# Kernel optimization log

Measured on AMD Instinct MI355X. Metric: run time of the kernel, lower is better.

The kernel has to match this reference:

```python
import jax, jax.numpy as jnp
import numpy as np

N_DRUG = 572
D = 512
K = 64          # neighbor_sample_size
T = 30000       # tail entities
R = 200         # relations
MAX_DEG = 32    # padded invariant_adj neighbor count
EPS = 1e-5


def setup_inputs() -> dict:
    key = jax.random.key(0)
    ks = jax.random.split(key, 10)
    return {
        "drug_embed_W": jax.random.normal(ks[0], (N_DRUG, D), jnp.float32),
        "rela_embed_W": jax.random.normal(ks[1], (R, D), jnp.float32),
        "ent_embed_W": jax.random.normal(ks[2], (T, D), jnp.float32),
        "Wa": jax.random.normal(ks[3], (D, D), jnp.float32) / np.float32(np.sqrt(D)),
        "lin_W": jax.random.normal(ks[4], (2 * D, D), jnp.float32) / np.float32(np.sqrt(2 * D)),
        "lin_b": jnp.zeros((D,), jnp.float32),
        "gamma": jnp.ones((D,), jnp.float32),
        "beta": jnp.zeros((D,), jnp.float32),
        "drug_name": jnp.arange(N_DRUG, dtype=jnp.int64 if jax.config.jax_enable_x64 else jnp.int32),
        "adj_tail": jax.random.randint(ks[5], (N_DRUG, K), 0, T),
        "adj_relation": jax.random.randint(ks[6], (N_DRUG, K), 0, R),
        "nbr_idx": jax.random.randint(ks[7], (N_DRUG, MAX_DEG), 0, N_DRUG),
        "nbr_deg": jax.random.randint(ks[8], (N_DRUG,), 0, MAX_DEG),
        "epoch": 2,
    }


def _forward(drug_embed_W, rela_embed_W, ent_embed_W, Wa, lin_W, lin_b, gamma, beta,
             drug_name, adj_tail, adj_relation, nbr_idx, nbr_deg, epoch):
    drug_e = drug_embed_W[drug_name]          # [N, D]
    rela = rela_embed_W[adj_relation]         # [N, K, D]
    ent = ent_embed_W[adj_tail]               # [N, K, D]

    # relation-aware attention over sampled neighbors (AttentionLayer)
    q = drug_e @ Wa                           # [N, D]
    scores = jnp.einsum('nd,nkd->nk', q, rela) * (1.0 / np.float32(np.sqrt(D)))
    attn = jax.nn.softmax(scores, axis=1)     # [N, K]
    agg = jnp.einsum('nk,nkd->nd', attn, ent) # [N, D]

    # Linear1: Linear(2D->D) + ReLU + BatchNorm1d (training-mode batch stats)
    h = jnp.concatenate([agg, drug_e], axis=1) @ lin_W + lin_b
    h = jax.nn.relu(h)
    mean = jnp.mean(h, axis=0)
    var = jnp.var(h, axis=0)                  # biased, as torch BN normalization
    drug_f = (h - mean) * jax.lax.rsqrt(var + EPS) * gamma + beta

    if epoch > 1:
        # sequential per-node neighbor-mean smoothing (in-place semantics)
        mask = (jnp.arange(MAX_DEG)[None, :] < nbr_deg[:, None])  # [N, MAX_DEG]

        def step(f, i):
            pos = nbr_idx[i]
            m = mask[i][:, None].astype(f.dtype)
            s = jnp.sum(f[pos] * m, axis=0)
            deg = nbr_deg[i]
            avg = s / jnp.maximum(deg, 1).astype(f.dtype)
            new = jnp.where(deg > 0, (avg + f[i]) * 0.5, f[i])
            return f.at[i].set(new), None

        drug_f, _ = jax.lax.scan(step, drug_f, jnp.arange(N_DRUG))
    return drug_f


def reference(drug_embed_W, rela_embed_W, ent_embed_W, Wa, lin_W, lin_b, gamma, beta,
              drug_name, adj_tail, adj_relation, nbr_idx, nbr_deg, epoch):
    return _forward(drug_embed_W, rela_embed_W, ent_embed_W, Wa, lin_W, lin_b, gamma, beta,
                    drug_name, adj_tail, adj_relation, nbr_idx, nbr_deg, epoch)
```

## Files before the change

kernel.cpp:

```cpp
#include <hip/hip_runtime.h>

#define N_DRUG 572
#define DIM 512
#define KNBR 64
#define MAXDEG 32
#define FS 17
#define MN (N_DRUG * DIM)
#define LSTR 68

__global__ __launch_bounds__(256) void gemm_kernel(
    const float* __restrict__ drugW, const int* __restrict__ drug_name,
    const float* __restrict__ agg, const float* __restrict__ B,
    float* __restrict__ C, int M, int Kc, int mode)
{
    __shared__ float As[2][32 * LSTR];
    __shared__ float Bs[2][32 * LSTR];
    const int t   = threadIdx.x;
    const int tn  = t & 15, tm = t >> 4;
    const int arow = t & 63, akq = (t >> 6) * 8;
    const int brow = t >> 3, bcq = (t & 7) * 8;
    const int c0  = blockIdx.x * 64;
    const int r0  = blockIdx.y * 64;
    const int ks0 = blockIdx.z * Kc;
    const int nsteps = Kc >> 5;
    const int row = r0 + arow;
    const bool aval = row < M;
    const int dn = aval ? drug_name[row] : 0;
    const float* __restrict__ drow = drugW + (size_t)dn * 512;
    const float* __restrict__ grow = agg + (size_t)row * 512;

    float av[8], bv[8];
    float acc[4][4] = {{0.f}};

    {
        const int k = ks0 + akq;
        if (aval) {
            const float* src = (mode == 1) ? ((k < 512) ? (grow + k) : (drow + (k - 512)))
                                           : (drow + k);
            const float4 x = ((const float4*)src)[0];
            const float4 y = ((const float4*)src)[1];
            av[0]=x.x; av[1]=x.y; av[2]=x.z; av[3]=x.w;
            av[4]=y.x; av[5]=y.y; av[6]=y.z; av[7]=y.w;
        } else {
            #pragma unroll
            for (int j = 0; j < 8; ++j) av[j] = 0.f;
        }
        const float* bsrc = B + (size_t)(ks0 + brow) * 512 + c0 + bcq;
        const float4 x = ((const float4*)bsrc)[0];
        const float4 y = ((const float4*)bsrc)[1];
        bv[0]=x.x; bv[1]=x.y; bv[2]=x.z; bv[3]=x.w;
        bv[4]=y.x; bv[5]=y.y; bv[6]=y.z; bv[7]=y.w;
    }
    #pragma unroll
    for (int i = 0; i < 8; ++i) As[0][(akq + i) * LSTR + arow] = av[i];
    *(float4*)&Bs[0][brow * LSTR + bcq]     = make_float4(bv[0], bv[1], bv[2], bv[3]);
    *(float4*)&Bs[0][brow * LSTR + bcq + 4] = make_float4(bv[4], bv[5], bv[6], bv[7]);
    __syncthreads();

    int p = 0;
    for (int s = 0; s < nsteps; ++s) {
        const bool more = (s + 1) < nsteps;
        if (more) {
            const int k = ks0 + (s + 1) * 32 + akq;
            if (aval) {
                const float* src = (mode == 1) ? ((k < 512) ? (grow + k) : (drow + (k - 512)))
                                               : (drow + k);
                const float4 x = ((const float4*)src)[0];
                const float4 y = ((const float4*)src)[1];
                av[0]=x.x; av[1]=x.y; av[2]=x.z; av[3]=x.w;
                av[4]=y.x; av[5]=y.y; av[6]=y.z; av[7]=y.w;
            }
            const float* bsrc = B + (size_t)(ks0 + (s + 1) * 32 + brow) * 512 + c0 + bcq;
            const float4 x = ((const float4*)bsrc)[0];
            const float4 y = ((const float4*)bsrc)[1];
            bv[0]=x.x; bv[1]=x.y; bv[2]=x.z; bv[3]=x.w;
            bv[4]=y.x; bv[5]=y.y; bv[6]=y.z; bv[7]=y.w;
        }
        #pragma unroll
        for (int kk = 0; kk < 32; ++kk) {
            const float4 a = *(const float4*)&As[p][kk * LSTR + tm * 4];
            const float4 b = *(const float4*)&Bs[p][kk * LSTR + tn * 4];
            const float ar[4] = {a.x, a.y, a.z, a.w};
            const float br[4] = {b.x, b.y, b.z, b.w};
            #pragma unroll
            for (int i = 0; i < 4; ++i)
                #pragma unroll
                for (int j = 0; j < 4; ++j)
                    acc[i][j] = fmaf(ar[i], br[j], acc[i][j]);
        }
        __syncthreads();
        if (more) {
            const int q2 = p ^ 1;
            #pragma unroll
            for (int i = 0; i < 8; ++i) As[q2][(akq + i) * LSTR + arow] = av[i];
            *(float4*)&Bs[q2][brow * LSTR + bcq]     = make_float4(bv[0], bv[1], bv[2], bv[3]);
            *(float4*)&Bs[q2][brow * LSTR + bcq + 4] = make_float4(bv[4], bv[5], bv[6], bv[7]);
            __syncthreads();
            p = q2;
        }
    }

    float* __restrict__ Cp = C + (size_t)blockIdx.z * MN;
    #pragma unroll
    for (int i = 0; i < 4; ++i) {
        const int r = r0 + tm * 4 + i;
        if (r < M)
            *(float4*)&Cp[(size_t)r * 512 + c0 + tn * 4] =
                make_float4(acc[i][0], acc[i][1], acc[i][2], acc[i][3]);
    }
}

__global__ __launch_bounds__(256) void attn_kernel(
    const float* __restrict__ relaW, const float* __restrict__ entW,
    const int* __restrict__ adj_tail, const int* __restrict__ adj_rel,
    const float* __restrict__ q, int skq, float* __restrict__ agg)
{
    const int n = blockIdx.x;
    const int t = threadIdx.x;
    const int lane = t & 63;
    const int w = t >> 6;
    __shared__ float sc[64];
    __shared__ int tails[64];
    __shared__ int rels[64];
    if (t < 64) { tails[t] = adj_tail[n * 64 + t]; rels[t] = adj_rel[n * 64 + t]; }

    float qv[8];
    {
        const float* qp = q + (size_t)n * 512 + lane * 8;
        float4 x = ((const float4*)qp)[0], y = ((const float4*)qp)[1];
        qv[0]=x.x; qv[1]=x.y; qv[2]=x.z; qv[3]=x.w;
        qv[4]=y.x; qv[5]=y.y; qv[6]=y.z; qv[7]=y.w;
        if (skq == 2) {
            const float* qp2 = qp + MN;
            float4 x2 = ((const float4*)qp2)[0], y2 = ((const float4*)qp2)[1];
            qv[0]+=x2.x; qv[1]+=x2.y; qv[2]+=x2.z; qv[3]+=x2.w;
            qv[4]+=y2.x; qv[5]+=y2.y; qv[6]+=y2.z; qv[7]+=y2.w;
        }
    }
    __syncthreads();

    #pragma unroll 4
    for (int kk = 0; kk < 16; ++kk) {
        const int k = w * 16 + kk;
        const float4* p = (const float4*)(relaW + (size_t)rels[k] * 512 + lane * 8);
        float4 x = p[0], y = p[1];
        float s = 0.f;
        s = fmaf(qv[0], x.x, s); s = fmaf(qv[1], x.y, s);
        s = fmaf(qv[2], x.z, s); s = fmaf(qv[3], x.w, s);
        s = fmaf(qv[4], y.x, s); s = fmaf(qv[5], y.y, s);
        s = fmaf(qv[6], y.z, s); s = fmaf(qv[7], y.w, s);
        #pragma unroll
        for (int off = 32; off >= 1; off >>= 1) s += __shfl_xor(s, off, 64);
        if (lane == 0) sc[k] = s * 0.0441941738241592f;
    }
    __syncthreads();

    if (w == 0) {
        float s = sc[lane];
        float m = s;
        #pragma unroll
        for (int off = 32; off >= 1; off >>= 1) m = fmaxf(m, __shfl_xor(m, off, 64));
        const float e = __expf(s - m);
        float sum = e;
        #pragma unroll
        for (int off = 32; off >= 1; off >>= 1) sum += __shfl_xor(sum, off, 64);
        sc[lane] = e / sum;
    }
    __syncthreads();

    float a0 = 0.f, a1 = 0.f;
    const int d2 = t * 2;
    #pragma unroll 8
    for (int k = 0; k < 64; ++k) {
        const float ak = sc[k];
        const float2 u = *(const float2*)(entW + (size_t)tails[k] * 512 + d2);
        a0 = fmaf(ak, u.x, a0);
        a1 = fmaf(ak, u.y, a1);
    }
    ((float2*)(agg + (size_t)n * 512))[t] = make_float2(a0, a1);
}

__global__ __launch_bounds__(512) void scan_kernel(
    float* hout, const float* __restrict__ hsrc, int nh,
    const float* __restrict__ linb,
    const float* __restrict__ gamma, const float* __restrict__ beta,
    const int* __restrict__ nbr_idx, const int* __restrict__ nbr_deg,
    const int* __restrict__ epoch)
{
    __shared__ float fs[(N_DRUG + 1) * FS];
    __shared__ int   offs[N_DRUG * MAXDEG];
    __shared__ float2 ivw[N_DRUG];
    __shared__ int   mxs[N_DRUG];
    __shared__ float part[2][32][16];
    __shared__ float bnp[2][16];
    __shared__ int   genext[2];
    __shared__ int   ge0s;

    const int t  = threadIdx.x;
    const int c  = t & 15;
    const int h  = (t >> 4) & 1;
    const int j  = t >> 5;
    const int rr = t >> 4;
    const int c0 = blockIdx.x * 16;

    for (int i = t; i < N_DRUG; i += 512) {
        const int d = nbr_deg[i];
        ivw[i] = (d > 0) ? make_float2(0.5f / (float)d, 0.5f) : make_float2(0.f, 1.f);
        const int4* np = (const int4*)&nbr_idx[i * MAXDEG];
        int4* op = (int4*)&offs[i * MAXDEG];
        int mx = -1;
        #pragma unroll
        for (int u = 0; u < 8; ++u) {
            int4 qq = np[u];
            const int b = u * 4;
            qq.x = (b + 0 < d) ? qq.x : N_DRUG;
            qq.y = (b + 1 < d) ? qq.y : N_DRUG;
            qq.z = (b + 2 < d) ? qq.z : N_DRUG;
            qq.w = (b + 3 < d) ? qq.w : N_DRUG;
            mx = max(mx, (qq.x < i) ? qq.x : -1);
            mx = max(mx, (qq.y < i) ? qq.y : -1);
            mx = max(mx, (qq.z < i) ? qq.z : -1);
            mx = max(mx, (qq.w < i) ? qq.w : -1);
            op[u] = qq;
        }
        mxs[i] = mx;
    }

    {
        const float bb = linb[c0 + c];
        float sl = 0.f, ql = 0.f;
        for (int r = rr; r < N_DRUG; r += 32) {
            const float* hp = hsrc + (size_t)r * DIM + c0 + c;
            float v = hp[0];
            for (int pt = 1; pt < nh; ++pt) v += hp[(size_t)pt * MN];
            v = fmaxf(v + bb, 0.f);
            fs[r * FS + c] = v;
            sl += v;
            ql = fmaf(v, v, ql);
        }
        part[0][rr][c] = sl;
        part[1][rr][c] = ql;
    }
    if (t < FS) fs[N_DRUG * FS + t] = 0.f;
    __syncthreads();

    if (t < 16) {
        float s = 0.f, sq = 0.f;
        #pragma unroll
        for (int k = 0; k < 32; ++k) { s += part[0][k][t]; sq += part[1][k][t]; }
        const float mean = s * (1.f / N_DRUG);
        const float var = sq * (1.f / N_DRUG) - mean * mean;
        const float rstd = rsqrtf(var + 1e-5f);
        const float scl = gamma[c0 + t] * rstd;
        bnp[0][t] = scl;
        bnp[1][t] = beta[c0 + t] - mean * scl;
    }
    if ((t >> 6) == 7) {
        const int l = t & 63;
        const int jj = 1 + l;
        const bool flag = (l >= 15) || (jj >= N_DRUG) || (mxs[min(jj, N_DRUG - 1)] >= 0);
        const unsigned long long b = __ballot(flag) & 0xFFFFULL;
        if (l == 0) ge0s = 1 + (int)__builtin_ctzll(b);
    }
    __syncthreads();

    {
        const float scl = bnp[0][c];
        const float shf = bnp[1][c];
        for (int r = rr; r < N_DRUG; r += 32)
            fs[r * FS + c] = fmaf(fs[r * FS + c], scl, shf);
    }
    __syncthreads();

    if (epoch[0] > 1) {
        int gs = 0, ge = ge0s;
        int4 o0, o1, o2, o3;
        {
            const int4* p = (const int4*)&offs[min(j, N_DRUG - 1) * MAXDEG + h * 16];
            o0 = p[0]; o1 = p[1]; o2 = p[2]; o3 = p[3];
        }
        int par = 0;
        while (gs < N_DRUG) {
            const bool pred = (gs + j) < ge;
            float s0 = 0.f, s1 = 0.f, s2 = 0.f, s3 = 0.f;
#define GATH4(Q) { s0 += fs[Q.x * FS + c]; s1 += fs[Q.y * FS + c]; \
                   s2 += fs[Q.z * FS + c]; s3 += fs[Q.w * FS + c]; }
            if (pred) { GATH4(o0) GATH4(o1) GATH4(o2) GATH4(o3) }
#undef GATH4
            int4 n0, n1, n2, n3;
            {
                const int4* p = (const int4*)&offs[min(ge + j, N_DRUG - 1) * MAXDEG + h * 16];
                n0 = p[0]; n1 = p[1]; n2 = p[2]; n3 = p[3];
            }
            float nv = 0.f;
            if (pred) {
                const float cur = fs[(gs + j) * FS + c];
                const float2 iw = ivw[gs + j];
                float sh = (s0 + s1) + (s2 + s3);
                sh += __shfl_xor(sh, 16, 64);
                nv = fmaf(sh, iw.x, cur * iw.y);
            }
            if ((t >> 6) == 7) {
                const int l = t & 63;
                const int jj = ge + 1 + l;
                const bool flag = (l >= 15) || (jj >= N_DRUG) ||
                                  (mxs[min(jj, N_DRUG - 1)] >= ge);
                const unsigned long long b = __ballot(flag) & 0xFFFFULL;
                if (l == 0) genext[par] = ge + 1 + (int)__builtin_ctzll(b);
            }
            __syncthreads();
            if (pred && h == 0) fs[(gs + j) * FS + c] = nv;
            __syncthreads();
            gs = ge;
            ge = genext[par];
            par ^= 1;
            o0 = n0; o1 = n1; o2 = n2; o3 = n3;
        }
    }
    __syncthreads();

    for (int r = rr; r < N_DRUG; r += 32)
        hout[(size_t)r * DIM + c0 + c] = fs[r * FS + c];
}

extern "C" void kernel_launch(void* const* d_in, const int* in_sizes, int n_in,
                              void* d_out, int out_size, void* d_ws, size_t ws_size,
                              hipStream_t stream)
{
    const float* drugW = (const float*)d_in[0];
    const float* relaW = (const float*)d_in[1];
    const float* entW  = (const float*)d_in[2];
    const float* Wa    = (const float*)d_in[3];
    const float* linW  = (const float*)d_in[4];
    const float* linb  = (const float*)d_in[5];
    const float* gamma = (const float*)d_in[6];
    const float* beta  = (const float*)d_in[7];
    const int* drug_name = (const int*)d_in[8];
    const int* adj_tail  = (const int*)d_in[9];
    const int* adj_rel   = (const int*)d_in[10];
    const int* nbr_idx   = (const int*)d_in[11];
    const int* nbr_deg   = (const int*)d_in[12];
    const int* epoch     = (const int*)d_in[13];

    float* ws = (float*)d_ws;
    float* out = (float*)d_out;

    const bool big = ws_size >= (size_t)7 * MN * sizeof(float);
    const int skq = big ? 2 : 1;
    const int skh = big ? 4 : 1;
    float* q   = ws;
    float* agg = ws + (size_t)(big ? 2 : 1) * MN;
    float* hp  = big ? (ws + (size_t)3 * MN) : out;

    gemm_kernel<<<dim3(8, 9, skq), 256, 0, stream>>>(
        drugW, drug_name, nullptr, Wa, q, N_DRUG, 512 / skq, 0);
    attn_kernel<<<N_DRUG, 256, 0, stream>>>(
        relaW, entW, adj_tail, adj_rel, q, skq, agg);
    gemm_kernel<<<dim3(8, 9, skh), 256, 0, stream>>>(
        drugW, drug_name, agg, linW, hp, N_DRUG, 1024 / skh, 1);
    scan_kernel<<<32, 512, 0, stream>>>(
        out, hp, skh, linb, gamma, beta, nbr_idx, nbr_deg, epoch);
}
```

Measured before the change: 226.1 us.

## Fuse all stages into one persistent kernel with grid barriers

```diff
diff --git a/kernel.cpp b/kernel.cpp
--- a/kernel.cpp
+++ b/kernel.cpp
@@ -2,26 +2,50 @@
 
 #define N_DRUG 572
 #define DIM 512
-#define KNBR 64
 #define MAXDEG 32
-#define FS 17
 #define MN (N_DRUG * DIM)
 #define LSTR 68
-
-__global__ __launch_bounds__(256) void gemm_kernel(
+#define FSW 9
+#define NBLK 256
+
+struct GemmS { float As[2][32 * LSTR]; float Bs[2][32 * LSTR]; };
+struct AttnS { float sc[64]; int tails[64]; int rels[64]; };
+struct ScanS {
+    float fs[(N_DRUG + 1) * FSW];
+    float fspad[3];
+    alignas(16) unsigned short offs[N_DRUG * MAXDEG];
+    float inv[N_DRUG];
+    unsigned short mxs[N_DRUG];
+    float part[2][32][8];
+    float bnp[2][8];
+    int genext[2];
+    int ge0;
+};
+union SmemU { GemmS g; AttnS a; ScanS s; };
+
+__device__ __forceinline__ void gridbar(int* cnt, int id) {
+    __syncthreads();
+    if (threadIdx.x == 0) {
+        __hip_atomic_fetch_add(&cnt[id], 1, __ATOMIC_ACQ_REL, __HIP_MEMORY_SCOPE_AGENT);
+        while (__hip_atomic_load(&cnt[id], __ATOMIC_RELAXED, __HIP_MEMORY_SCOPE_AGENT) < NBLK)
+            __builtin_amdgcn_s_sleep(8);
+        __builtin_amdgcn_fence(__ATOMIC_ACQUIRE, "agent");
+    }
+    __syncthreads();
+}
+
+__device__ void gemm_tile(GemmS& g,
     const float* __restrict__ drugW, const int* __restrict__ drug_name,
     const float* __restrict__ agg, const float* __restrict__ B,
-    float* __restrict__ C, int M, int Kc, int mode)
+    float* __restrict__ C, int M, int Kc, int mode, int bx, int by, int bz)
 {
-    __shared__ float As[2][32 * LSTR];
-    __shared__ float Bs[2][32 * LSTR];
-    const int t   = threadIdx.x;
-    const int tn  = t & 15, tm = t >> 4;
+    __syncthreads();
+    const int t = threadIdx.x;
+    const int tn = t & 15, tm = t >> 4;
     const int arow = t & 63, akq = (t >> 6) * 8;
     const int brow = t >> 3, bcq = (t & 7) * 8;
-    const int c0  = blockIdx.x * 64;
-    const int r0  = blockIdx.y * 64;
-    const int ks0 = blockIdx.z * Kc;
+    const int c0 = bx * 64, r0 = by * 64;
+    const int ks0 = bz * Kc;
     const int nsteps = Kc >> 5;
     const int row = r0 + arow;
     const bool aval = row < M;
@@ -52,9 +76,9 @@
         bv[4]=y.x; bv[5]=y.y; bv[6]=y.z; bv[7]=y.w;
     }
     #pragma unroll
-    for (int i = 0; i < 8; ++i) As[0][(akq + i) * LSTR + arow] = av[i];
-    *(float4*)&Bs[0][brow * LSTR + bcq]     = make_float4(bv[0], bv[1], bv[2], bv[3]);
-    *(float4*)&Bs[0][brow * LSTR + bcq + 4] = make_float4(bv[4], bv[5], bv[6], bv[7]);
+    for (int i = 0; i < 8; ++i) g.As[0][(akq + i) * LSTR + arow] = av[i];
+    *(float4*)&g.Bs[0][brow * LSTR + bcq]     = make_float4(bv[0], bv[1], bv[2], bv[3]);
+    *(float4*)&g.Bs[0][brow * LSTR + bcq + 4] = make_float4(bv[4], bv[5], bv[6], bv[7]);
     __syncthreads();
 
     int p = 0;
@@ -78,8 +102,8 @@
         }
         #pragma unroll
         for (int kk = 0; kk < 32; ++kk) {
-            const float4 a = *(const float4*)&As[p][kk * LSTR + tm * 4];
-            const float4 b = *(const float4*)&Bs[p][kk * LSTR + tn * 4];
+            const float4 a = *(const float4*)&g.As[p][kk * LSTR + tm * 4];
+            const float4 b = *(const float4*)&g.Bs[p][kk * LSTR + tn * 4];
             const float ar[4] = {a.x, a.y, a.z, a.w};
             const float br[4] = {b.x, b.y, b.z, b.w};
             #pragma unroll
@@ -92,15 +116,15 @@
         if (more) {
             const int q2 = p ^ 1;
             #pragma unroll
-            for (int i = 0; i < 8; ++i) As[q2][(akq + i) * LSTR + arow] = av[i];
-            *(float4*)&Bs[q2][brow * LSTR + bcq]     = make_float4(bv[0], bv[1], bv[2], bv[3]);
-            *(float4*)&Bs[q2][brow * LSTR + bcq + 4] = make_float4(bv[4], bv[5], bv[6], bv[7]);
+            for (int i = 0; i < 8; ++i) g.As[q2][(akq + i) * LSTR + arow] = av[i];
+            *(float4*)&g.Bs[q2][brow * LSTR + bcq]     = make_float4(bv[0], bv[1], bv[2], bv[3]);
+            *(float4*)&g.Bs[q2][brow * LSTR + bcq + 4] = make_float4(bv[4], bv[5], bv[6], bv[7]);
             __syncthreads();
             p = q2;
         }
     }
 
-    float* __restrict__ Cp = C + (size_t)blockIdx.z * MN;
+    float* __restrict__ Cp = C + (size_t)bz * MN;
     #pragma unroll
     for (int i = 0; i < 4; ++i) {
         const int r = r0 + tm * 4 + i;
@@ -110,29 +134,26 @@
     }
 }
 
-__global__ __launch_bounds__(256) void attn_kernel(
+__device__ void attn_one(AttnS& a,
     const float* __restrict__ relaW, const float* __restrict__ entW,
     const int* __restrict__ adj_tail, const int* __restrict__ adj_rel,
-    const float* __restrict__ q, int skq, float* __restrict__ agg)
+    const float* __restrict__ qb, int skq, float* __restrict__ agg, int n)
 {
-    const int n = blockIdx.x;
     const int t = threadIdx.x;
     const int lane = t & 63;
     const int w = t >> 6;
-    __shared__ float sc[64];
-    __shared__ int tails[64];
-    __shared__ int rels[64];
-    if (t < 64) { tails[t] = adj_tail[n * 64 + t]; rels[t] = adj_rel[n * 64 + t]; }
+    __syncthreads();
+    if (t < 64) { a.tails[t] = adj_tail[n * 64 + t]; a.rels[t] = adj_rel[n * 64 + t]; }
 
     float qv[8];
     {
-        const float* qp = q + (size_t)n * 512 + lane * 8;
+        const float* qp = qb + (size_t)n * 512 + lane * 8;
         float4 x = ((const float4*)qp)[0], y = ((const float4*)qp)[1];
         qv[0]=x.x; qv[1]=x.y; qv[2]=x.z; qv[3]=x.w;
         qv[4]=y.x; qv[5]=y.y; qv[6]=y.z; qv[7]=y.w;
-        if (skq == 2) {
-            const float* qp2 = qp + MN;
-            float4 x2 = ((const float4*)qp2)[0], y2 = ((const float4*)qp2)[1];
+        for (int pt = 1; pt < skq; ++pt) {
+            const float* q2 = qp + (size_t)pt * MN;
+            float4 x2 = ((const float4*)q2)[0], y2 = ((const float4*)q2)[1];
             qv[0]+=x2.x; qv[1]+=x2.y; qv[2]+=x2.z; qv[3]+=x2.w;
             qv[4]+=y2.x; qv[5]+=y2.y; qv[6]+=y2.z; qv[7]+=y2.w;
         }
@@ -142,7 +163,7 @@
     #pragma unroll 4
     for (int kk = 0; kk < 16; ++kk) {
         const int k = w * 16 + kk;
-        const float4* p = (const float4*)(relaW + (size_t)rels[k] * 512 + lane * 8);
+        const float4* p = (const float4*)(relaW + (size_t)a.rels[k] * 512 + lane * 8);
         float4 x = p[0], y = p[1];
         float s = 0.f;
         s = fmaf(qv[0], x.x, s); s = fmaf(qv[1], x.y, s);
@@ -151,12 +172,12 @@
         s = fmaf(qv[6], y.z, s); s = fmaf(qv[7], y.w, s);
         #pragma unroll
         for (int off = 32; off >= 1; off >>= 1) s += __shfl_xor(s, off, 64);
-        if (lane == 0) sc[k] = s * 0.0441941738241592f;
+        if (lane == 0) a.sc[k] = s * 0.0441941738241592f;
     }
     __syncthreads();
 
     if (w == 0) {
-        float s = sc[lane];
+        float s = a.sc[lane];
         float m = s;
         #pragma unroll
         for (int off = 32; off >= 1; off >>= 1) m = fmaxf(m, __shfl_xor(m, off, 64));
@@ -164,7 +185,7 @@
         float sum = e;
         #pragma unroll
         for (int off = 32; off >= 1; off >>= 1) sum += __shfl_xor(sum, off, 64);
-        sc[lane] = e / sum;
+        a.sc[lane] = e / sum;
     }
     __syncthreads();
 
@@ -172,155 +193,184 @@
     const int d2 = t * 2;
     #pragma unroll 8
     for (int k = 0; k < 64; ++k) {
-        const float ak = sc[k];
-        const float2 u = *(const float2*)(entW + (size_t)tails[k] * 512 + d2);
+        const float ak = a.sc[k];
+        const float2 u = *(const float2*)(entW + (size_t)a.tails[k] * 512 + d2);
         a0 = fmaf(ak, u.x, a0);
         a1 = fmaf(ak, u.y, a1);
     }
     ((float2*)(agg + (size_t)n * 512))[t] = make_float2(a0, a1);
 }
 
-__global__ __launch_bounds__(512) void scan_kernel(
-    float* hout, const float* __restrict__ hsrc, int nh,
-    const float* __restrict__ linb,
+__global__ __launch_bounds__(256, 1) void mega_kernel(
+    const float* __restrict__ drugW, const float* __restrict__ relaW,
+    const float* __restrict__ entW, const float* __restrict__ Wa,
+    const float* __restrict__ linW, const float* __restrict__ linb,
     const float* __restrict__ gamma, const float* __restrict__ beta,
-    const int* __restrict__ nbr_idx, const int* __restrict__ nbr_deg,
-    const int* __restrict__ epoch)
+    const int* __restrict__ drug_name, const int* __restrict__ adj_tail,
+    const int* __restrict__ adj_rel, const int* __restrict__ nbr_idx,
+    const int* __restrict__ nbr_deg, const int* __restrict__ epoch,
+    int skq, int skh, int* cnt, float* q, float* agg, float* hbuf,
+    float* __restrict__ out)
 {
-    __shared__ float fs[(N_DRUG + 1) * FS];
-    __shared__ int   offs[N_DRUG * MAXDEG];
-    __shared__ float2 ivw[N_DRUG];
-    __shared__ int   mxs[N_DRUG];
-    __shared__ float part[2][32][16];
-    __shared__ float bnp[2][16];
-    __shared__ int   genext[2];
-    __shared__ int   ge0s;
-
-    const int t  = threadIdx.x;
-    const int c  = t & 15;
-    const int h  = (t >> 4) & 1;
-    const int j  = t >> 5;
-    const int rr = t >> 4;
-    const int c0 = blockIdx.x * 16;
-
-    for (int i = t; i < N_DRUG; i += 512) {
-        const int d = nbr_deg[i];
-        ivw[i] = (d > 0) ? make_float2(0.5f / (float)d, 0.5f) : make_float2(0.f, 1.f);
-        const int4* np = (const int4*)&nbr_idx[i * MAXDEG];
-        int4* op = (int4*)&offs[i * MAXDEG];
-        int mx = -1;
-        #pragma unroll
-        for (int u = 0; u < 8; ++u) {
-            int4 qq = np[u];
-            const int b = u * 4;
-            qq.x = (b + 0 < d) ? qq.x : N_DRUG;
-            qq.y = (b + 1 < d) ? qq.y : N_DRUG;
-            qq.z = (b + 2 < d) ? qq.z : N_DRUG;
-            qq.w = (b + 3 < d) ? qq.w : N_DRUG;
-            mx = max(mx, (qq.x < i) ? qq.x : -1);
-            mx = max(mx, (qq.y < i) ? qq.y : -1);
-            mx = max(mx, (qq.z < i) ? qq.z : -1);
-            mx = max(mx, (qq.w < i) ? qq.w : -1);
-            op[u] = qq;
-        }
-        mxs[i] = mx;
-    }
-
+    __shared__ SmemU sm;
+    const int blk = blockIdx.x;
+    const int t = threadIdx.x;
+
+    for (int job = blk; job < 72 * skq; job += NBLK) {
+        const int bz = job / 72, rem = job % 72;
+        gemm_tile(sm.g, drugW, drug_name, q , Wa, q,
+                  N_DRUG, 512 / skq, 0, rem % 8, rem / 8, bz);
+    }
+    gridbar(cnt, 0);
+
+    for (int n = blk; n < N_DRUG; n += NBLK)
+        attn_one(sm.a, relaW, entW, adj_tail, adj_rel, q, skq, agg, n);
+    gridbar(cnt, 1);
+
+    for (int job = blk; job < 72 * skh; job += NBLK) {
+        const int bz = job / 72, rem = job % 72;
+        gemm_tile(sm.g, drugW, drug_name, agg, linW, hbuf,
+                  N_DRUG, 1024 / skh, 1, rem % 8, rem / 8, bz);
+    }
+    gridbar(cnt, 2);
+
+    if (blk >= 64) return;
+    __syncthreads();
     {
-        const float bb = linb[c0 + c];
-        float sl = 0.f, ql = 0.f;
-        for (int r = rr; r < N_DRUG; r += 32) {
-            const float* hp = hsrc + (size_t)r * DIM + c0 + c;
-            float v = hp[0];
-            for (int pt = 1; pt < nh; ++pt) v += hp[(size_t)pt * MN];
-            v = fmaxf(v + bb, 0.f);
-            fs[r * FS + c] = v;
-            sl += v;
-            ql = fmaf(v, v, ql);
-        }
-        part[0][rr][c] = sl;
-        part[1][rr][c] = ql;
-    }
-    if (t < FS) fs[N_DRUG * FS + t] = 0.f;
-    __syncthreads();
-
-    if (t < 16) {
-        float s = 0.f, sq = 0.f;
-        #pragma unroll
-        for (int k = 0; k < 32; ++k) { s += part[0][k][t]; sq += part[1][k][t]; }
-        const float mean = s * (1.f / N_DRUG);
-        const float var = sq * (1.f / N_DRUG) - mean * mean;
-        const float rstd = rsqrtf(var + 1e-5f);
-        const float scl = gamma[c0 + t] * rstd;
-        bnp[0][t] = scl;
-        bnp[1][t] = beta[c0 + t] - mean * scl;
-    }
-    if ((t >> 6) == 7) {
-        const int l = t & 63;
-        const int jj = 1 + l;
-        const bool flag = (l >= 15) || (jj >= N_DRUG) || (mxs[min(jj, N_DRUG - 1)] >= 0);
-        const unsigned long long b = __ballot(flag) & 0xFFFFULL;
-        if (l == 0) ge0s = 1 + (int)__builtin_ctzll(b);
-    }
-    __syncthreads();
-
-    {
-        const float scl = bnp[0][c];
-        const float shf = bnp[1][c];
+        ScanS& S = sm.s;
+        const int c8 = t & 7;
+        const int rr = t >> 3;
+        const int h  = (t >> 3) & 1;
+        const int j  = t >> 4;
+        const int c0 = blk * 8;
+
+        for (int i = t; i < N_DRUG; i += 256) {
+            const int d = nbr_deg[i];
+            S.inv[i] = (d > 0) ? 0.5f / (float)d : 0.f;
+            const int4* np = (const int4*)&nbr_idx[i * MAXDEG];
+            unsigned* op = (unsigned*)&S.offs[i * MAXDEG];
+            int mx = -1;
+            #pragma unroll
+            for (int u = 0; u < 8; ++u) {
+                int4 qq = np[u];
+                const int b = u * 4;
+                qq.x = (b + 0 < d) ? qq.x : N_DRUG;
+                qq.y = (b + 1 < d) ? qq.y : N_DRUG;
+                qq.z = (b + 2 < d) ? qq.z : N_DRUG;
+                qq.w = (b + 3 < d) ? qq.w : N_DRUG;
+                mx = max(mx, (qq.x < i) ? qq.x : -1);
+                mx = max(mx, (qq.y < i) ? qq.y : -1);
+                mx = max(mx, (qq.z < i) ? qq.z : -1);
+                mx = max(mx, (qq.w < i) ? qq.w : -1);
+                op[2 * u]     = (unsigned)(qq.x & 0xffff) | ((unsigned)qq.y << 16);
+                op[2 * u + 1] = (unsigned)(qq.z & 0xffff) | ((unsigned)qq.w << 16);
+            }
+            S.mxs[i] = (unsigned short)(mx + 1);
+        }
+        {
+            const float bb = linb[c0 + c8];
+            float sl = 0.f, ql = 0.f;
+            for (int r = rr; r < N_DRUG; r += 32) {
+                const float* hp = hbuf + (size_t)r * DIM + c0 + c8;
+                float v = hp[0];
+                for (int pt = 1; pt < skh; ++pt) v += hp[(size_t)pt * MN];
+                v = fmaxf(v + bb, 0.f);
+                S.fs[r * FSW + c8] = v;
+                sl += v;
+                ql = fmaf(v, v, ql);
+            }
+            S.part[0][rr][c8] = sl;
+            S.part[1][rr][c8] = ql;
+        }
+        if (t < FSW) S.fs[N_DRUG * FSW + t] = 0.f;
+        __syncthreads();
+
+        if (t < 8) {
+            float s = 0.f, sq = 0.f;
+            #pragma unroll
+            for (int k = 0; k < 32; ++k) { s += S.part[0][k][t]; sq += S.part[1][k][t]; }
+            const float mean = s * (1.f / N_DRUG);
+            const float var = sq * (1.f / N_DRUG) - mean * mean;
+            const float rstd = rsqrtf(var + 1e-5f);
+            const float scl = gamma[c0 + t] * rstd;
+            S.bnp[0][t] = scl;
+            S.bnp[1][t] = beta[c0 + t] - mean * scl;
+        }
+        if ((t >> 6) == 3) {
+            const int l = t & 63;
+            const int jj = 1 + l;
+            const bool flag = (l >= 15) || (jj >= N_DRUG) ||
+                              ((int)S.mxs[min(jj, N_DRUG - 1)] > 0);
+            const unsigned long long b = __ballot(flag) & 0xFFFFULL;
+            if (l == 0) S.ge0 = 1 + (int)__builtin_ctzll(b);
+        }
+        __syncthreads();
+
+        {
+            const float scl = S.bnp[0][c8];
+            const float shf = S.bnp[1][c8];
+            for (int r = rr; r < N_DRUG; r += 32)
+                S.fs[r * FSW + c8] = fmaf(S.fs[r * FSW + c8], scl, shf);
+        }
+        __syncthreads();
+
+        if (epoch[0] > 1) {
+            int gs = 0, ge = S.ge0, par = 0;
+            uint4 ca, cb;
+            {
+                const uint4* p = (const uint4*)&S.offs[min(j, N_DRUG - 1) * MAXDEG + h * 16];
+                ca = p[0]; cb = p[1];
+            }
+            while (gs < N_DRUG) {
+                const bool pred = (gs + j) < ge;
+                float sh = 0.f;
+                if (pred) {
+                    float s0 = 0.f, s1 = 0.f, s2 = 0.f, s3 = 0.f;
+#define G2(W) { s0 += S.fs[(W & 0xffffu) * FSW + c8]; s1 += S.fs[(W >> 16) * FSW + c8]; }
+#define G4(Q) { G2(Q.x) unsigned w2_##Q = 0; (void)w2_##Q; }
+                    G2(ca.x) G2(ca.y); s2 += 0.f; s3 += 0.f;
+                    G2(ca.z) G2(ca.w)
+                    G2(cb.x) G2(cb.y)
+                    G2(cb.z) G2(cb.w)
+#undef G4
+#undef G2
+                    sh = (s0 + s1) + (s2 + s3);
+                }
+                uint4 na, nb;
+                {
+                    const uint4* p = (const uint4*)&S.offs[min(ge + j, N_DRUG - 1) * MAXDEG + h * 16];
+                    na = p[0]; nb = p[1];
+                }
+                float nv = 0.f;
+                if (pred) {
+                    const float cur = S.fs[(gs + j) * FSW + c8];
+                    const float iv = S.inv[gs + j];
+                    const float wg = (iv == 0.f) ? 1.f : 0.5f;
+                    float sx = sh + __shfl_xor(sh, 8, 64);
+                    nv = fmaf(sx, iv, cur * wg);
+                }
+                if ((t >> 6) == 3) {
+                    const int l = t & 63;
+                    const int jj = ge + 1 + l;
+                    const bool flag = (l >= 15) || (jj >= N_DRUG) ||
+                                      ((int)S.mxs[min(jj, N_DRUG - 1)] > ge);
+                    const unsigned long long b = __ballot(flag) & 0xFFFFULL;
+                    if (l == 0) S.genext[par] = ge + 1 + (int)__builtin_ctzll(b);
+                }
+                __syncthreads();
+                if (pred && h == 0) S.fs[(gs + j) * FSW + c8] = nv;
+                __syncthreads();
+                gs = ge;
+                ge = S.genext[par];
+                par ^= 1;
+                ca = na; cb = nb;
+            }
+        }
+        __syncthreads();
+
         for (int r = rr; r < N_DRUG; r += 32)
-            fs[r * FS + c] = fmaf(fs[r * FS + c], scl, shf);
-    }
-    __syncthreads();
-
-    if (epoch[0] > 1) {
-        int gs = 0, ge = ge0s;
-        int4 o0, o1, o2, o3;
-        {
-            const int4* p = (const int4*)&offs[min(j, N_DRUG - 1) * MAXDEG + h * 16];
-            o0 = p[0]; o1 = p[1]; o2 = p[2]; o3 = p[3];
-        }
-        int par = 0;
-        while (gs < N_DRUG) {
-            const bool pred = (gs + j) < ge;
-            float s0 = 0.f, s1 = 0.f, s2 = 0.f, s3 = 0.f;
-#define GATH4(Q) { s0 += fs[Q.x * FS + c]; s1 += fs[Q.y * FS + c]; \
-                   s2 += fs[Q.z * FS + c]; s3 += fs[Q.w * FS + c]; }
-            if (pred) { GATH4(o0) GATH4(o1) GATH4(o2) GATH4(o3) }
-#undef GATH4
-            int4 n0, n1, n2, n3;
-            {
-                const int4* p = (const int4*)&offs[min(ge + j, N_DRUG - 1) * MAXDEG + h * 16];
-                n0 = p[0]; n1 = p[1]; n2 = p[2]; n3 = p[3];
-            }
-            float nv = 0.f;
-            if (pred) {
-                const float cur = fs[(gs + j) * FS + c];
-                const float2 iw = ivw[gs + j];
-                float sh = (s0 + s1) + (s2 + s3);
-                sh += __shfl_xor(sh, 16, 64);
-                nv = fmaf(sh, iw.x, cur * iw.y);
-            }
-            if ((t >> 6) == 7) {
-                const int l = t & 63;
-                const int jj = ge + 1 + l;
-                const bool flag = (l >= 15) || (jj >= N_DRUG) ||
-                                  (mxs[min(jj, N_DRUG - 1)] >= ge);
-                const unsigned long long b = __ballot(flag) & 0xFFFFULL;
-                if (l == 0) genext[par] = ge + 1 + (int)__builtin_ctzll(b);
-            }
-            __syncthreads();
-            if (pred && h == 0) fs[(gs + j) * FS + c] = nv;
-            __syncthreads();
-            gs = ge;
-            ge = genext[par];
-            par ^= 1;
-            o0 = n0; o1 = n1; o2 = n2; o3 = n3;
-        }
-    }
-    __syncthreads();
-
-    for (int r = rr; r < N_DRUG; r += 32)
-        hout[(size_t)r * DIM + c0 + c] = fs[r * FS + c];
+            out[(size_t)r * DIM + c0 + c8] = S.fs[r * FSW + c8];
+    }
 }
 
 extern "C" void kernel_launch(void* const* d_in, const int* in_sizes, int n_in,
@@ -342,22 +392,19 @@
     const int* nbr_deg   = (const int*)d_in[12];
     const int* epoch     = (const int*)d_in[13];
 
-    float* ws = (float*)d_ws;
+    int* cnt = (int*)d_ws;
+    float* base = (float*)d_ws + 16;
+    const bool big = ws_size >= (size_t)(7 * MN + 16) * sizeof(float);
+    const int skq = big ? 2 : 1;
+    const int skh = big ? 4 : 2;
+    float* q   = base;
+    float* agg = q + (size_t)skq * MN;
+    float* hb  = agg + (size_t)MN;
     float* out = (float*)d_out;
 
-    const bool big = ws_size >= (size_t)7 * MN * sizeof(float);
-    const int skq = big ? 2 : 1;
-    const int skh = big ? 4 : 1;
-    float* q   = ws;
-    float* agg = ws + (size_t)(big ? 2 : 1) * MN;
-    float* hp  = big ? (ws + (size_t)3 * MN) : out;
-
-    gemm_kernel<<<dim3(8, 9, skq), 256, 0, stream>>>(
-        drugW, drug_name, nullptr, Wa, q, N_DRUG, 512 / skq, 0);
-    attn_kernel<<<N_DRUG, 256, 0, stream>>>(
-        relaW, entW, adj_tail, adj_rel, q, skq, agg);
-    gemm_kernel<<<dim3(8, 9, skh), 256, 0, stream>>>(
-        drugW, drug_name, agg, linW, hp, N_DRUG, 1024 / skh, 1);
-    scan_kernel<<<32, 512, 0, stream>>>(
-        out, hp, skh, linb, gamma, beta, nbr_idx, nbr_deg, epoch);
+    hipMemsetAsync(d_ws, 0, 64, stream);
+    mega_kernel<<<NBLK, 256, 0, stream>>>(
+        drugW, relaW, entW, Wa, linW, linb, gamma, beta,
+        drug_name, adj_tail, adj_rel, nbr_idx, nbr_deg, epoch,
+        skq, skh, cnt, q, agg, hb, out);
 }
```

Result: slower. 334.0 us (+47.7%).
